# Kernel optimization log

Measured on AMD Instinct MI355X. Metric: run time of the kernel, lower is better.

Reference implementation:

```python
import jax, jax.numpy as jnp
import numpy as np

HEADS = 12
DIM_HEAD = 64
SCALE = DIM_HEAD ** -0.5

def setup_inputs() -> dict:
    key = jax.random.key(0)
    k1, k2, k3, k4 = jax.random.split(key, 4)
    dim, inner = 768, HEADS * DIM_HEAD
    x = jax.random.normal(k1, (4, 2048, dim), dtype=jnp.float32)
    w_qkv = jax.random.normal(k2, (dim, 3 * inner), dtype=jnp.float32) * (dim ** -0.5)
    w_out = jax.random.normal(k3, (inner, dim), dtype=jnp.float32) * (inner ** -0.5)
    b_out = jax.random.normal(k4, (dim,), dtype=jnp.float32) * 0.02
    return {"x": x, "w_qkv": w_qkv, "w_out": w_out, "b_out": b_out}

def reference(x, w_qkv, w_out, b_out):
    B, N, _ = x.shape
    qkv = jnp.einsum('bnd,de->bne', x, w_qkv)  # [B,N,3*inner]
    q, k, v = jnp.split(qkv, 3, axis=-1)
    # b n (h d) -> b h n d
    split_heads = lambda t: t.reshape(B, N, HEADS, DIM_HEAD).transpose(0, 2, 1, 3)
    q, k, v = split_heads(q), split_heads(k), split_heads(v)
    dots = jnp.einsum('bhnd,bhmd->bhnm', q, k) * SCALE  # [B,H,N,N]
    attn = jax.nn.softmax(dots, axis=-1)
    out = jnp.einsum('bhnm,bhmd->bhnd', attn, v)
    out = out.transpose(0, 2, 1, 3).reshape(B, N, HEADS * DIM_HEAD)  # b h n d -> b n (h d)
    return jnp.einsum('bne,ed->bnd', out, w_out) + b_out
```

## Files before the change

### kernel.cpp

```cpp
#include <hip/hip_runtime.h>
#include <stdint.h>

typedef unsigned short ushort_t;
typedef __attribute__((ext_vector_type(8))) short short8;
typedef __attribute__((ext_vector_type(4))) short s16x4;
typedef __attribute__((ext_vector_type(4))) float f32x4;
typedef __attribute__((ext_vector_type(2))) uint32_t u32x2;

#define BATCH 4
#define SEQ 2048
#define DMODEL 768
#define NH 12
#define HD 64
#define QKV3 2304
#define NHEADS 48
#define SCALE_Q 0.18033688011112042f

__device__ __forceinline__ ushort_t f2bf(float f) {
    union { float f; uint32_t u; } v; v.f = f;
    uint32_t u = v.u;
    u += 0x7FFF + ((u >> 16) & 1);
    return (ushort_t)(u >> 16);
}

__device__ __forceinline__ uint32_t pack_bf16(float a, float b) {
#if __has_builtin(__builtin_amdgcn_cvt_pk_bf16_f32)
    typedef __attribute__((ext_vector_type(2))) __bf16 bf16x2;
    bf16x2 r = __builtin_amdgcn_cvt_pk_bf16_f32(a, b);
    return __builtin_bit_cast(uint32_t, r);
#else
    return ((uint32_t)f2bf(b) << 16) | (uint32_t)f2bf(a);
#endif
}

typedef __attribute__((address_space(1))) uint32_t as1_u32;
typedef __attribute__((address_space(3))) uint32_t as3_u32;
__device__ __forceinline__ void async16(void* lds, const void* gsrc) {
    __builtin_amdgcn_global_load_lds((as1_u32*)gsrc, (as3_u32*)lds, 16, 0, 0);
}

__device__ __forceinline__ void wait_vm_lgkm0() {
    __builtin_amdgcn_s_waitcnt(0x0070);
}

__device__ __forceinline__ f32x4 mfma16x16x16bf16(s16x4 a, s16x4 b, f32x4 c) {
#if __has_builtin(__builtin_amdgcn_mfma_f32_16x16x16bf16_1k)
    return __builtin_amdgcn_mfma_f32_16x16x16bf16_1k(a, b, c, 0, 0, 0);
#else
    f32x4 d;
    asm volatile("v_mfma_f32_16x16x16_bf16 %0, %1, %2, %3"
                 : "=&v"(d) : "v"(a), "v"(b), "0"(c));
    return d;
#endif
}

__global__ __launch_bounds__(256) void cvt_bf16(
    const float* __restrict__ in, ushort_t* __restrict__ out) {
    int i = blockIdx.x * 256 + threadIdx.x;
    float4 v = *(const float4*)(in + (size_t)i * 4);
    ushort4 o; o.x = f2bf(v.x); o.y = f2bf(v.y); o.z = f2bf(v.z); o.w = f2bf(v.w);
    *(ushort4*)(out + (size_t)i * 4) = o;
}

__global__ __launch_bounds__(256) void transpose_f32_bf16(
    const float* __restrict__ in, ushort_t* __restrict__ out, int R, int C) {
    __shared__ ushort_t t[64][72];
    const int tid = threadIdx.x;
    const int r0 = blockIdx.y * 64, c0 = blockIdx.x * 64;
#pragma unroll
    for (int i = 0; i < 4; i++) {
        int idx = tid + i * 256;
        int row = idx >> 4, c4 = (idx & 15) * 4;
        float4 v = *(const float4*)(in + (size_t)(r0 + row) * C + c0 + c4);
        ushort4 o; o.x = f2bf(v.x); o.y = f2bf(v.y); o.z = f2bf(v.z); o.w = f2bf(v.w);
        *(ushort4*)&t[row][c4] = o;
    }
    __syncthreads();
#pragma unroll
    for (int i = 0; i < 2; i++) {
        int idx = tid + i * 256;
        int oc = idx >> 3, g8 = (idx & 7) * 8;
        ushort_t tmp[8];
#pragma unroll
        for (int e = 0; e < 8; e++) tmp[e] = t[g8 + e][oc];
        *(short8*)(out + (size_t)(c0 + oc) * R + r0 + g8) = *(const short8*)tmp;
    }
}

__global__ __launch_bounds__(256, 2) void gemm_qkv(
    const ushort_t* __restrict__ A, const ushort_t* __restrict__ B,
    ushort_t* __restrict__ qkv, ushort_t* __restrict__ vT) {
    __shared__ ushort_t As[128 * 64];
    __shared__ ushort_t Bs[128 * 64];

    const int tid = threadIdx.x;
    const int m0 = blockIdx.y * 128, n0 = blockIdx.x * 128;
    const int lane = tid & 63, w = tid >> 6;
    const int wm = w >> 1, wn = w & 1;
    const int l16 = lane & 15, quad = lane >> 4;

    f32x4 acc[4][4];
#pragma unroll
    for (int i = 0; i < 4; i++)
#pragma unroll
        for (int j = 0; j < 4; j++) acc[i][j] = (f32x4){0.f, 0.f, 0.f, 0.f};

    int srow[4], scol[4];
#pragma unroll
    for (int j = 0; j < 4; j++) {
        int s = j * 256 + tid;
        srow[j] = s >> 3;
        scol[j] = ((s & 7) ^ (srow[j] & 7)) * 8;
    }
    const int swz0 = (quad ^ (l16 & 7)) * 8;
    const int swz1 = ((4 + quad) ^ (l16 & 7)) * 8;

    for (int kt = 0; kt < DMODEL; kt += 64) {
#pragma unroll
        for (int j = 0; j < 4; j++) {
            async16(&As[(j * 256 + w * 64) * 8],
                    A + (size_t)(m0 + srow[j]) * DMODEL + kt + scol[j]);
            async16(&Bs[(j * 256 + w * 64) * 8],
                    B + (size_t)(n0 + srow[j]) * DMODEL + kt + scol[j]);
        }
        wait_vm_lgkm0();
        __syncthreads();

        short8 a[4][2], b[4][2];
#pragma unroll
        for (int mi = 0; mi < 4; mi++) {
            int r = (wm * 64 + mi * 16 + l16) * 64;
            a[mi][0] = *(const short8*)&As[r + swz0];
            a[mi][1] = *(const short8*)&As[r + swz1];
        }
#pragma unroll
        for (int ni = 0; ni < 4; ni++) {
            int r = (wn * 64 + ni * 16 + l16) * 64;
            b[ni][0] = *(const short8*)&Bs[r + swz0];
            b[ni][1] = *(const short8*)&Bs[r + swz1];
        }
#pragma unroll
        for (int kk = 0; kk < 2; kk++)
#pragma unroll
            for (int mi = 0; mi < 4; mi++)
#pragma unroll
                for (int ni = 0; ni < 4; ni++)
                    acc[mi][ni] = __builtin_amdgcn_mfma_f32_16x16x32_bf16(
                        a[mi][kk], b[ni][kk], acc[mi][ni], 0, 0, 0);
        __syncthreads();
    }

#pragma unroll
    for (int ni = 0; ni < 4; ni++) {
        int nbase = n0 + wn * 64 + ni * 16;
        int which = nbase / DMODEL;
        int rem = nbase - which * DMODEL;
        int h = rem >> 6;
        int d = (rem & 63) + l16;
        if (which == 2) {
#pragma unroll
            for (int mi = 0; mi < 4; mi++) {
                int mg = m0 + wm * 64 + mi * 16 + quad * 4;
                int b_ = mg >> 11, ns = mg & 2047;
                u32x2 pk = {pack_bf16(acc[mi][ni][0], acc[mi][ni][1]),
                            pack_bf16(acc[mi][ni][2], acc[mi][ni][3])};
                *(u32x2*)(vT + ((size_t)(b_ * NH + h) * HD + d) * SEQ + ns) = pk;
            }
        } else {
            float scale = (which == 0) ? SCALE_Q : 1.0f;
#pragma unroll
            for (int mi = 0; mi < 4; mi++) {
#pragma unroll
                for (int r = 0; r < 4; r++) {
                    int mg = m0 + wm * 64 + mi * 16 + quad * 4 + r;
                    int b_ = mg >> 11, ns = mg & 2047;
                    size_t dst = (((size_t)(which * BATCH + b_) * NH + h) * SEQ + ns) * HD + d;
                    qkv[dst] = f2bf(acc[mi][ni][r] * scale);
                }
            }
        }
    }
}

__global__ __launch_bounds__(256, 3) void attn(
    const ushort_t* __restrict__ qkv, const ushort_t* __restrict__ vT,
    ushort_t* __restrict__ ao) {
    __shared__ ushort_t smem[16384];

    const int tid = threadIdx.x;
    const int bid = blockIdx.x;
    const int i = bid >> 3;
    const int bh = (bid & 7) + 8 * (i % 6);
    const int qt = i / 6;
    const int lane = tid & 63, w = tid >> 6;
    const int l16 = lane & 15, quad = lane >> 4;
    const int qh7 = l16 & 7, qhi = quad >> 1, qlo4 = (quad & 1) * 4;

    const ushort_t* qh = qkv + (size_t)bh * (SEQ * HD);
    const ushort_t* kh = qkv + (size_t)(NHEADS + bh) * (SEQ * HD);
    const ushort_t* vh = vT + (size_t)bh * (HD * SEQ);

    short8 aq[2][2];
#pragma unroll
    for (int mi = 0; mi < 2; mi++)
#pragma unroll
        for (int kk = 0; kk < 2; kk++) {
            int row = qt * 128 + w * 32 + mi * 16 + l16;
            aq[mi][kk] = *(const short8*)(qh + (size_t)row * HD + kk * 32 + quad * 8);
        }

    f32x4 lv[2];
    f32x4 O[4][2];
#pragma unroll
    for (int mi = 0; mi < 2; mi++) lv[mi] = (f32x4){0.f, 0.f, 0.f, 0.f};
#pragma unroll
    for (int nd = 0; nd < 4; nd++)
#pragma unroll
        for (int mi = 0; mi < 2; mi++) O[nd][mi] = (f32x4){0.f, 0.f, 0.f, 0.f};

    int srow[2], scol[2];
#pragma unroll
    for (int j = 0; j < 2; j++) {
        int s = j * 256 + tid;
        srow[j] = s >> 3;
        scol[j] = ((s & 7) ^ (srow[j] & 7)) * 8;
    }
    const int swz0 = (quad ^ qh7) * 8;
    const int swz1 = ((4 + quad) ^ qh7) * 8;

#pragma unroll
    for (int j = 0; j < 2; j++) {
        async16(&smem[(j * 256 + w * 64) * 8],
                kh + (size_t)srow[j] * HD + scol[j]);
        async16(&smem[4096 + (j * 256 + w * 64) * 8],
                vh + (size_t)srow[j] * SEQ + scol[j]);
    }

    const int NT = SEQ / 64;
    for (int t = 0; t < NT; t++) {
        wait_vm_lgkm0();
        __syncthreads();
        if (t + 1 < NT) {
            int nb = ((t + 1) & 1) * 8192, j1 = (t + 1) * 64;
#pragma unroll
            for (int j = 0; j < 2; j++) {
                async16(&smem[nb + (j * 256 + w * 64) * 8],
                        kh + (size_t)(j1 + srow[j]) * HD + scol[j]);
                async16(&smem[nb + 4096 + (j * 256 + w * 64) * 8],
                        vh + (size_t)srow[j] * SEQ + j1 + scol[j]);
            }
        }
        const ushort_t* Ks = smem + (t & 1) * 8192;
        const ushort_t* Vs = Ks + 4096;

#pragma unroll
        for (int ni = 0; ni < 4; ni++) {
            int r = (ni * 16 + l16) * 64;
            short8 ak0 = *(const short8*)&Ks[r + swz0];
            short8 ak1 = *(const short8*)&Ks[r + swz1];
            s16x4 bp[2];
#pragma unroll
            for (int mi = 0; mi < 2; mi++) {
                f32x4 s = __builtin_amdgcn_mfma_f32_16x16x32_bf16(
                    ak0, aq[mi][0], (f32x4){0.f, 0.f, 0.f, 0.f}, 0, 0, 0);
                s = __builtin_amdgcn_mfma_f32_16x16x32_bf16(
                    ak1, aq[mi][1], s, 0, 0, 0);
                f32x4 p;
#pragma unroll
                for (int rr = 0; rr < 4; rr++)
                    p[rr] = __builtin_amdgcn_exp2f(s[rr]);
                lv[mi] += p;
                bp[mi] = __builtin_bit_cast(
                    s16x4, (u32x2){pack_bf16(p[0], p[1]), pack_bf16(p[2], p[3])});
            }
#pragma unroll
            for (int nd = 0; nd < 4; nd++) {
                int vrow = nd * 16 + l16;
                s16x4 av = *(const s16x4*)&Vs[vrow * 64 +
                                              (((ni * 2 + qhi) ^ qh7) * 8) + qlo4];
#pragma unroll
                for (int mi = 0; mi < 2; mi++)
                    O[nd][mi] = mfma16x16x16bf16(av, bp[mi], O[nd][mi]);
            }
        }
    }

    float inv[2];
#pragma unroll
    for (int mi = 0; mi < 2; mi++) {
        float l = (lv[mi][0] + lv[mi][1]) + (lv[mi][2] + lv[mi][3]);
        l += __shfl_xor(l, 16, 64);
        l += __shfl_xor(l, 32, 64);
        inv[mi] = __builtin_amdgcn_rcpf(l);
    }
    wait_vm_lgkm0();
    __syncthreads();
    ushort_t* Lt = smem;
#pragma unroll
    for (int mi = 0; mi < 2; mi++)
#pragma unroll
        for (int nd = 0; nd < 4; nd++) {
            int row = w * 32 + mi * 16 + l16;
            int col = nd * 16 + quad * 4;
            uint32_t d0 = pack_bf16(O[nd][mi][0] * inv[mi], O[nd][mi][1] * inv[mi]);
            uint32_t d1 = pack_bf16(O[nd][mi][2] * inv[mi], O[nd][mi][3] * inv[mi]);
            *(u32x2*)&Lt[row * 72 + col] = (u32x2){d0, d1};
        }
    __syncthreads();

    const int b_ = bh / NH, h = bh % NH;
#pragma unroll
    for (int i2 = 0; i2 < 4; i2++) {
        int idx = tid + i2 * 256;
        int row = idx >> 3, c8 = (idx & 7) * 8;
        short8 vv = *(const short8*)&Lt[row * 72 + c8];
        *(short8*)(ao + ((size_t)(b_ * SEQ + qt * 128 + row)) * DMODEL +
                   h * HD + c8) = vv;
    }
}

__global__ __launch_bounds__(256, 2) void gemm_out(
    const ushort_t* __restrict__ A, const ushort_t* __restrict__ B,
    const float* __restrict__ bias, float* __restrict__ out) {
    __shared__ ushort_t As[128 * 64];
    __shared__ ushort_t Bs[128 * 64];

    const int tid = threadIdx.x;
    const int m0 = blockIdx.y * 128, n0 = blockIdx.x * 128;
    const int lane = tid & 63, w = tid >> 6;
    const int wm = w >> 1, wn = w & 1;
    const int l16 = lane & 15, quad = lane >> 4;

    f32x4 acc[4][4];
#pragma unroll
    for (int i = 0; i < 4; i++)
#pragma unroll
        for (int j = 0; j < 4; j++) acc[i][j] = (f32x4){0.f, 0.f, 0.f, 0.f};

    int srow[4], scol[4];
#pragma unroll
    for (int j = 0; j < 4; j++) {
        int s = j * 256 + tid;
        srow[j] = s >> 3;
        scol[j] = ((s & 7) ^ (srow[j] & 7)) * 8;
    }
    const int swz0 = (quad ^ (l16 & 7)) * 8;
    const int swz1 = ((4 + quad) ^ (l16 & 7)) * 8;

    for (int kt = 0; kt < DMODEL; kt += 64) {
#pragma unroll
        for (int j = 0; j < 4; j++) {
            async16(&As[(j * 256 + w * 64) * 8],
                    A + (size_t)(m0 + srow[j]) * DMODEL + kt + scol[j]);
            async16(&Bs[(j * 256 + w * 64) * 8],
                    B + (size_t)(n0 + srow[j]) * DMODEL + kt + scol[j]);
        }
        wait_vm_lgkm0();
        __syncthreads();

        short8 a[4][2], b[4][2];
#pragma unroll
        for (int mi = 0; mi < 4; mi++) {
            int r = (wm * 64 + mi * 16 + l16) * 64;
            a[mi][0] = *(const short8*)&As[r + swz0];
            a[mi][1] = *(const short8*)&As[r + swz1];
        }
#pragma unroll
        for (int ni = 0; ni < 4; ni++) {
            int r = (wn * 64 + ni * 16 + l16) * 64;
            b[ni][0] = *(const short8*)&Bs[r + swz0];
            b[ni][1] = *(const short8*)&Bs[r + swz1];
        }
#pragma unroll
        for (int kk = 0; kk < 2; kk++)
#pragma unroll
            for (int mi = 0; mi < 4; mi++)
#pragma unroll
                for (int ni = 0; ni < 4; ni++)
                    acc[mi][ni] = __builtin_amdgcn_mfma_f32_16x16x32_bf16(
                        a[mi][kk], b[ni][kk], acc[mi][ni], 0, 0, 0);
        __syncthreads();
    }

#pragma unroll
    for (int ni = 0; ni < 4; ni++) {
        int ng = n0 + wn * 64 + ni * 16 + l16;
        float bv = bias[ng];
#pragma unroll
        for (int mi = 0; mi < 4; mi++) {
#pragma unroll
            for (int r = 0; r < 4; r++) {
                int mg = m0 + wm * 64 + mi * 16 + quad * 4 + r;
                out[(size_t)mg * DMODEL + ng] = acc[mi][ni][r] + bv;
            }
        }
    }
}

extern "C" void kernel_launch(void* const* d_in, const int* in_sizes, int n_in,
                              void* d_out, int out_size, void* d_ws, size_t ws_size,
                              hipStream_t stream) {
    const float* x     = (const float*)d_in[0];
    const float* w_qkv = (const float*)d_in[1];
    const float* w_out = (const float*)d_in[2];
    const float* b_out = (const float*)d_in[3];
    float* out = (float*)d_out;

    ushort_t* xb  = (ushort_t*)d_ws;
    ushort_t* wqT = xb  + (size_t)8192 * 768;
    ushort_t* woT = wqT + (size_t)QKV3 * 768;
    ushort_t* qkv = woT + (size_t)768 * 768;
    ushort_t* vT  = qkv + (size_t)3 * NHEADS * SEQ * HD;
    ushort_t* ao  = vT  + (size_t)NHEADS * HD * SEQ;

    cvt_bf16<<<dim3((8192 * 768) / 4 / 256), 256, 0, stream>>>(x, xb);
    transpose_f32_bf16<<<dim3(QKV3 / 64, DMODEL / 64), 256, 0, stream>>>(
        w_qkv, wqT, DMODEL, QKV3);
    transpose_f32_bf16<<<dim3(DMODEL / 64, DMODEL / 64), 256, 0, stream>>>(
        w_out, woT, DMODEL, DMODEL);

    gemm_qkv<<<dim3(QKV3 / 128, (BATCH * SEQ) / 128), 256, 0, stream>>>(
        xb, wqT, qkv, vT);

    attn<<<dim3(NHEADS * (SEQ / 128)), 256, 0, stream>>>(qkv, vT, ao);

    gemm_out<<<dim3(DMODEL / 128, (BATCH * SEQ) / 128), 256, 0, stream>>>(
        ao, woT, b_out, out);
}
```

Baseline: 218.5 us.

## Triple-buffer K/V tiles in attention and batch QK MFMAs before softmax

The attention kernel moves from double to triple buffering in LDS. It prefetches two tiles ahead and waits with a partial vmcnt, so one tile's loads can stay in flight across the barrier. The inner loop is also reordered: it loads all K fragments first, issues every QK MFMA, applies exp2 in bulk, then runs the PV MFMAs, which gives the scheduler more independent work. LDS use grows from 32KB to 48KB per block, which may reduce the 3-blocks-per-CU occupancy target, and the larger live S/ak arrays raise register pressure.

```diff
diff --git a/kernel.cpp b/kernel.cpp
--- a/kernel.cpp
+++ b/kernel.cpp
@@ -185,7 +185,7 @@
 __global__ __launch_bounds__(256, 3) void attn(
     const ushort_t* __restrict__ qkv, const ushort_t* __restrict__ vT,
     ushort_t* __restrict__ ao) {
-    __shared__ ushort_t smem[16384];
+    __shared__ ushort_t smem[3 * 8192];
 
     const int tid = threadIdx.x;
     const int bid = blockIdx.x;
@@ -229,19 +229,29 @@
     const int swz1 = ((4 + quad) ^ qh7) * 8;
 
 #pragma unroll
-    for (int j = 0; j < 2; j++) {
-        async16(&smem[(j * 256 + w * 64) * 8],
-                kh + (size_t)srow[j] * HD + scol[j]);
-        async16(&smem[4096 + (j * 256 + w * 64) * 8],
-                vh + (size_t)srow[j] * SEQ + scol[j]);
+    for (int pt = 0; pt < 2; pt++) {
+        int nb = pt * 8192, j1 = pt * 64;
+#pragma unroll
+        for (int j = 0; j < 2; j++) {
+            async16(&smem[nb + (j * 256 + w * 64) * 8],
+                    kh + (size_t)(j1 + srow[j]) * HD + scol[j]);
+            async16(&smem[nb + 4096 + (j * 256 + w * 64) * 8],
+                    vh + (size_t)srow[j] * SEQ + j1 + scol[j]);
+        }
     }
 
     const int NT = SEQ / 64;
+    int buf = 0;
+    int pf = 2;
     for (int t = 0; t < NT; t++) {
-        wait_vm_lgkm0();
-        __syncthreads();
-        if (t + 1 < NT) {
-            int nb = ((t + 1) & 1) * 8192, j1 = (t + 1) * 64;
+        if (t == NT - 1)
+            __builtin_amdgcn_s_waitcnt(0x0070);
+        else
+            __builtin_amdgcn_s_waitcnt(0x0074);
+        asm volatile("s_barrier" ::: "memory");
+
+        if (t + 2 < NT) {
+            int nb = pf * 8192, j1 = (t + 2) * 64;
 #pragma unroll
             for (int j = 0; j < 2; j++) {
                 async16(&smem[nb + (j * 256 + w * 64) * 8],
@@ -250,34 +260,54 @@
                         vh + (size_t)srow[j] * SEQ + j1 + scol[j]);
             }
         }
-        const ushort_t* Ks = smem + (t & 1) * 8192;
+        const ushort_t* Ks = smem + buf * 8192;
         const ushort_t* Vs = Ks + 4096;
-
+        buf = (buf == 2) ? 0 : buf + 1;
+        pf = (pf == 2) ? 0 : pf + 1;
+
+        f32x4 S[4][2];
+        short8 ak[4][2];
 #pragma unroll
         for (int ni = 0; ni < 4; ni++) {
             int r = (ni * 16 + l16) * 64;
-            short8 ak0 = *(const short8*)&Ks[r + swz0];
-            short8 ak1 = *(const short8*)&Ks[r + swz1];
-            s16x4 bp[2];
+            ak[ni][0] = *(const short8*)&Ks[r + swz0];
+            ak[ni][1] = *(const short8*)&Ks[r + swz1];
+        }
+#pragma unroll
+        for (int ni = 0; ni < 4; ni++)
 #pragma unroll
             for (int mi = 0; mi < 2; mi++) {
                 f32x4 s = __builtin_amdgcn_mfma_f32_16x16x32_bf16(
-                    ak0, aq[mi][0], (f32x4){0.f, 0.f, 0.f, 0.f}, 0, 0, 0);
-                s = __builtin_amdgcn_mfma_f32_16x16x32_bf16(
-                    ak1, aq[mi][1], s, 0, 0, 0);
+                    ak[ni][0], aq[mi][0], (f32x4){0.f, 0.f, 0.f, 0.f}, 0, 0, 0);
+                S[ni][mi] = __builtin_amdgcn_mfma_f32_16x16x32_bf16(
+                    ak[ni][1], aq[mi][1], s, 0, 0, 0);
+            }
+
+#pragma unroll
+        for (int mi = 0; mi < 2; mi++)
+#pragma unroll
+            for (int ni = 0; ni < 4; ni++) {
                 f32x4 p;
 #pragma unroll
                 for (int rr = 0; rr < 4; rr++)
-                    p[rr] = __builtin_amdgcn_exp2f(s[rr]);
+                    p[rr] = __builtin_amdgcn_exp2f(S[ni][mi][rr]);
+                S[ni][mi] = p;
                 lv[mi] += p;
+            }
+
+#pragma unroll
+        for (int kb = 0; kb < 4; kb++) {
+            s16x4 bp[2];
+#pragma unroll
+            for (int mi = 0; mi < 2; mi++)
                 bp[mi] = __builtin_bit_cast(
-                    s16x4, (u32x2){pack_bf16(p[0], p[1]), pack_bf16(p[2], p[3])});
-            }
+                    s16x4, (u32x2){pack_bf16(S[kb][mi][0], S[kb][mi][1]),
+                                   pack_bf16(S[kb][mi][2], S[kb][mi][3])});
 #pragma unroll
             for (int nd = 0; nd < 4; nd++) {
                 int vrow = nd * 16 + l16;
                 s16x4 av = *(const s16x4*)&Vs[vrow * 64 +
-                                              (((ni * 2 + qhi) ^ qh7) * 8) + qlo4];
+                                              (((kb * 2 + qhi) ^ qh7) * 8) + qlo4];
 #pragma unroll
                 for (int mi = 0; mi < 2; mi++)
                     O[nd][mi] = mfma16x16x16bf16(av, bp[mi], O[nd][mi]);
@@ -294,7 +324,7 @@
         inv[mi] = __builtin_amdgcn_rcpf(l);
     }
     wait_vm_lgkm0();
-    __syncthreads();
+    asm volatile("s_barrier" ::: "memory");
     ushort_t* Lt = smem;
 #pragma unroll
     for (int mi = 0; mi < 2; mi++)
@@ -306,7 +336,8 @@
             uint32_t d1 = pack_bf16(O[nd][mi][2] * inv[mi], O[nd][mi][3] * inv[mi]);
             *(u32x2*)&Lt[row * 72 + col] = (u32x2){d0, d1};
         }
-    __syncthreads();
+    wait_vm_lgkm0();
+    asm volatile("s_barrier" ::: "memory");
 
     const int b_ = bh / NH, h = bh % NH;
 #pragma unroll
```

After: 222.2 us. Within noise of the previous version (+1.7%).
